# Kernel optimization log

Measured on AMD Instinct MI355X. Metric: run time of the kernel, lower is better.

The kernel has to match this reference:

```python
import jax, jax.numpy as jnp
import numpy as np
from jax import lax

NUM_HEAD = 16; M = 2; N = 2; RP = 16; HNR = 8; WNR = 8; NUM_RATIO = 64
ED = 4096           # origin_embed_dim == resize_embed_dim
HD = 4              # head dim (= ED / (NUM_HEAD * 64))
R = 1024 // RP      # 64
THETA = 10.0


def conv2d(x, w, b, stride, pad):
    y = lax.conv_general_dilated(x, w, (stride, stride), ((pad, pad), (pad, pad)),
                                 dimension_numbers=('NCHW', 'OIHW', 'NCHW'))
    return y + b[None, :, None, None]


def layernorm(x, g, b):
    mu = jnp.mean(x, -1, keepdims=True)
    var = jnp.mean((x - mu) ** 2, -1, keepdims=True)
    return (x - mu) * lax.rsqrt(var + 1e-5) * g + b


def l2norm(x):
    n = jnp.sqrt(jnp.sum(x * x, -1, keepdims=True))
    return x / jnp.maximum(n, 1e-12)


def window_partition(x, m, n):
    B, C, H, W = x.shape
    Hp = ((H + m - 1) // m) * m
    Wp = ((W + n - 1) // n) * n
    x = jnp.pad(x, ((0, 0), (0, 0), (0, Hp - H), (0, Wp - W)))
    wh, ww = Hp // m, Wp // n
    x = x.reshape(B, C, m, wh, n, ww).transpose(0, 2, 4, 1, 3, 5).reshape(B * m * n, C, wh, ww)
    return x, (wh, ww), (Hp, Wp)


def window_reverse(x, m, n, paged_shape):
    Hp, Wp = paged_shape
    Bmn, C, wh, ww = x.shape
    B = Bmn // (m * n)
    return x.reshape(B, m, n, C, wh, ww).transpose(0, 3, 1, 4, 2, 5).reshape(B, C, Hp, Wp)


def rope_rotate(t, h, w, theta):
    # 2D axial RoPE over a (h, w) grid flattened row-major; head dim split
    # half for the h-axis and half for the w-axis, consecutive-pair rotation.
    d = t.shape[-1]; dh = d // 2
    freqs = 1.0 / (theta ** (jnp.arange(0, dh, 2, dtype=jnp.float32) / dh))
    px = jnp.repeat(jnp.arange(h, dtype=jnp.float32), w)
    py = jnp.tile(jnp.arange(w, dtype=jnp.float32), h)
    ang = jnp.concatenate([px[:, None] * freqs, py[:, None] * freqs], -1)  # (h*w, dh)
    cos, sin = jnp.cos(ang), jnp.sin(ang)
    tp = t.reshape(t.shape[:-1] + (dh, 2))
    tr = jnp.stack([tp[..., 0] * cos - tp[..., 1] * sin,
                    tp[..., 0] * sin + tp[..., 1] * cos], -1)
    return tr.reshape(t.shape)


def setup_inputs() -> dict:
    key = jax.random.key(0)
    ks = jax.random.split(key, 12)
    s = 0.05
    inp = {
        'x': jax.random.normal(ks[0], (1, 3, 8, 8), jnp.float32),
        'x_conv_w': jax.random.normal(ks[1], (64, 3, 3, 3), jnp.float32) * s,
        'x_conv_b': jnp.zeros((64,), jnp.float32),
        'r_conv_w': jax.random.normal(ks[2], (64, 3, 3, 3), jnp.float32) * s,
        'r_conv_b': jnp.zeros((64,), jnp.float32),
        'patch_w': jax.random.normal(ks[3], (ED, 64, RP, RP), jnp.float32) * s,
        'patch_b': jnp.zeros((ED,), jnp.float32),
        'b_proj_w': jax.random.normal(ks[4], (HD, HD), jnp.float32) * 0.5,
        'b_proj_b': jnp.zeros((HD,), jnp.float32),
        'q_proj_w': jax.random.normal(ks[5], (HD, HD), jnp.float32) * 0.5,
        'q_proj_b': jnp.zeros((HD,), jnp.float32),
        'norm_b_g': jnp.ones((HD,), jnp.float32),
        'norm_b_b': jnp.zeros((HD,), jnp.float32),
        'norm_q_g': jnp.ones((HD,), jnp.float32),
        'norm_q_b': jnp.zeros((HD,), jnp.float32),
        'q_attn_w': jax.random.normal(ks[6], (1, HD), jnp.float32) * 0.5,
        'q_attn_b': jnp.zeros((1,), jnp.float32),
        'pos': jax.random.normal(ks[7], (1, NUM_HEAD, 65536, HD), jnp.float32),
        'proj_w': jax.random.normal(ks[8], (ED, ED, 1, 1), jnp.float32) * s,
        'proj_b': jnp.zeros((ED,), jnp.float32),
    }
    return inp


def reference(x, x_conv_w, x_conv_b, r_conv_w, r_conv_b, patch_w, patch_b,
              b_proj_w, b_proj_b, q_proj_w, q_proj_b,
              norm_b_g, norm_b_b, norm_q_g, norm_q_b,
              q_attn_w, q_attn_b, pos, proj_w, proj_b):
    B, C, H, W = x.shape
    x_feat = conv2d(x, x_conv_w, x_conv_b, 1, 1)                     # (B,64,H,W)
    x_win, xws, x_shape = window_partition(x_feat, M, N)
    pad_h, pad_w = x_shape[0] - H, x_shape[1] - W
    xp = jnp.pad(x, ((0, 0), (0, 0), (0, pad_h), (0, pad_w)))
    res_x = jax.image.resize(xp, (B, 3, 1024, 1024), method='bilinear')
    res_x = conv2d(res_x, r_conv_w, r_conv_b, 1, 1)                  # (B,64,1024,1024)
    res_x_base = conv2d(res_x, patch_w, patch_b, RP, 0)              # (B,4096,64,64)
    C_idx = ED // NUM_RATIO                                          # 64
    rxr = res_x_base.reshape(B, C_idx, HNR, WNR, R, R)
    rxr = rxr.transpose(0, 1, 4, 2, 5, 3).reshape(B, C_idx, R * HNR, R * WNR)  # (B,64,512,512)
    rx_win, rws, rx_shape = window_partition(rxr, M, N)              # (B*4,64,256,256)
    xw = x_win.reshape(B * M * N, NUM_HEAD, -1, xws[0] * xws[1]).swapaxes(-2, -1)  # (B*4,16,Nb,4)
    rw = rx_win.reshape(B * M * N, NUM_HEAD, -1, rws[0] * rws[1]).swapaxes(-2, -1) # (B*4,16,Nq,4)
    b = layernorm(xw, norm_b_g, norm_b_b) @ b_proj_w.T + b_proj_b
    q = layernorm(rw, norm_q_g, norm_q_b) @ q_proj_w.T + q_proj_b
    b_norm = l2norm(b)
    gate = jax.nn.sigmoid(q @ q_attn_w.T + q_attn_b)                 # (B*4,16,Nq,1)
    q = l2norm(q * gate + pos * (1.0 - gate))
    q_rot = rope_rotate(q, rws[0], rws[1], THETA)
    b_rot = rope_rotate(b_norm, xws[0], xws[1], THETA)
    attn = jnp.einsum('bhqd,bhkd->bhqk', q_rot, b_rot)               # (B*4,16,Nq,Nb)
    out_win = attn @ b                                               # (B*4,16,Nq,4)
    out_win = out_win.swapaxes(-2, -1).reshape(B * M * N, -1, rws[0], rws[1])
    n_x = window_reverse(out_win, M, N, rx_shape)                    # (B,64,512,512)
    n_x = n_x.reshape(B, C_idx, R, HNR, R, WNR).transpose(0, 1, 3, 5, 2, 4).reshape(B, -1, R, R)
    x_final = conv2d(n_x + res_x_base, proj_w, proj_b, 1, 0)         # (B,4096,64,64)
    return (x_final, attn)
```

## Files before the change

### kernel.cpp

```cpp
#include <hip/hip_runtime.h>
#include <hip/hip_bf16.h>
#include <math.h>
#include <cstddef>

#define CB_F     2097152ull
#define BIASC_F  4194304ull
#define BBUF_F   4198400ull
#define BROT_F   4202496ull
#define P_F      4206592ull
#define PB_F     20983808ull
#define PRWB_F   29372416ull
#define ATTN_OFF 16777216ull

typedef __attribute__((ext_vector_type(8))) short bf16x8;
typedef __attribute__((ext_vector_type(4))) float f32x4;

#define GLOAD16(gsrc, ldst) \
  __builtin_amdgcn_global_load_lds((const __attribute__((address_space(1))) void*)(gsrc), \
                                   (__attribute__((address_space(3))) void*)(ldst), 16, 0, 0)

__global__ __launch_bounds__(256) void k_xmap_bchain(
    const float* __restrict__ x, __hip_bfloat16* __restrict__ Xmb,
    const float* __restrict__ xcw, const float* __restrict__ xcb,
    const float* __restrict__ bpw, const float* __restrict__ bpb,
    const float* __restrict__ nbg, const float* __restrict__ nbb,
    float* __restrict__ b_buf, float* __restrict__ b_rot)
{
    __shared__ float xs[3][8][8];
    int t = threadIdx.x;
    if (t < 192) xs[t / 64][(t / 8) % 8][t % 8] = x[t];
    __syncthreads();

    if (blockIdx.x < 4096) {
        int s = blockIdx.x, py = s >> 6, px = s & 63;
        __hip_bfloat16 out4[4];
        #pragma unroll
        for (int u = 0; u < 4; ++u) {
            int k = t * 4 + u;
            float val = 0.0f;
            if (k < 972) {
                int ci = k / 324, r = k % 324, m = r / 18, n = r % 18;
                int row = 16 * py + m - 1, col = 16 * px + n - 1;
                if (row >= 0 && row < 1024 && col >= 0 && col < 1024) {
                    float fu = (row + 0.5f) * 0.0078125f - 0.5f;
                    float fv = (col + 0.5f) * 0.0078125f - 0.5f;
                    float fi = floorf(fu), fj = floorf(fv);
                    float tu = fu - fi, tv = fv - fj;
                    int i0 = (int)fi, j0 = (int)fj;
                    int i0c = min(max(i0, 0), 7), i1c = min(max(i0 + 1, 0), 7);
                    int j0c = min(max(j0, 0), 7), j1c = min(max(j0 + 1, 0), 7);
                    val = (xs[ci][i0c][j0c] * (1.f - tv) + xs[ci][i0c][j1c] * tv) * (1.f - tu)
                        + (xs[ci][i1c][j0c] * (1.f - tv) + xs[ci][i1c][j1c] * tv) * tu;
                }
            }
            out4[u] = __float2bfloat16(val);
        }
        *(ushort4*)(Xmb + (size_t)s * 1024 + t * 4) = *(const ushort4*)out4;
        return;
    }

    __shared__ float xf[64][8][8];
    for (int o = t; o < 4096; o += 256) {
        int c = o >> 6, i = (o >> 3) & 7, j = o & 7;
        float acc = xcb[c];
        for (int ic = 0; ic < 3; ++ic)
            for (int ky = 0; ky < 3; ++ky)
                for (int kx = 0; kx < 3; ++kx) {
                    int ii = i - 1 + ky, jj = j - 1 + kx;
                    if (ii >= 0 && ii < 8 && jj >= 0 && jj < 8)
                        acc = fmaf(xs[ic][ii][jj], xcw[((c * 3 + ic) * 3 + ky) * 3 + kx], acc);
                }
        xf[c][i][j] = acc;
    }
    __syncthreads();
    for (int idx = t; idx < 1024; idx += 256) {
        int wi = idx >> 8, h = (idx >> 4) & 15, pp = idx & 15;
        int pr = pp >> 2, pc = pp & 3;
        int gi = 4 * (wi >> 1) + pr, gj = 4 * (wi & 1) + pc;
        float v[4];
        #pragma unroll
        for (int d = 0; d < 4; ++d) v[d] = xf[h * 4 + d][gi][gj];
        float mu = 0.25f * (v[0] + v[1] + v[2] + v[3]);
        float var = 0.25f * ((v[0]-mu)*(v[0]-mu) + (v[1]-mu)*(v[1]-mu) +
                             (v[2]-mu)*(v[2]-mu) + (v[3]-mu)*(v[3]-mu));
        float inv = rsqrtf(var + 1e-5f);
        float xh[4];
        #pragma unroll
        for (int d = 0; d < 4; ++d) xh[d] = (v[d] - mu) * inv * nbg[d] + nbb[d];
        float bv[4];
        #pragma unroll
        for (int d = 0; d < 4; ++d) {
            float a = bpb[d];
            #pragma unroll
            for (int e = 0; e < 4; ++e) a = fmaf(xh[e], bpw[d * 4 + e], a);
            bv[d] = a;
        }
        #pragma unroll
        for (int d = 0; d < 4; ++d) b_buf[idx * 4 + d] = bv[d];
        float nn = sqrtf(bv[0]*bv[0] + bv[1]*bv[1] + bv[2]*bv[2] + bv[3]*bv[3]);
        float in2 = 1.0f / fmaxf(nn, 1e-12f);
        float bn[4];
        #pragma unroll
        for (int d = 0; d < 4; ++d) bn[d] = bv[d] * in2;
        float s0, c0, s1, c1;
        sincosf((float)pr, &s0, &c0);
        sincosf((float)pc, &s1, &c1);
        b_rot[idx * 4 + 0] = bn[0] * c0 - bn[1] * s0;
        b_rot[idx * 4 + 1] = bn[0] * s0 + bn[1] * c0;
        b_rot[idx * 4 + 2] = bn[2] * c1 - bn[3] * s1;
        b_rot[idx * 4 + 3] = bn[2] * s1 + bn[3] * c1;
    }
}

__global__ __launch_bounds__(256) void k_cmat(
    const float* __restrict__ pw, const float* __restrict__ rcw,
    const float* __restrict__ pb, const float* __restrict__ rcb,
    __hip_bfloat16* __restrict__ Cb, float* __restrict__ biasc)
{
    __shared__ __attribute__((aligned(16))) float Dz[20 * 20 * 28];
    __shared__ float red[256];
    int co = blockIdx.x;
    const float* pwc = pw + (size_t)co * 16384;
    int t = threadIdx.x;

    for (int i = t; i < 11200; i += 256) Dz[i] = 0.0f;

    float D[27] = {};
    float bsum = 0.0f;
    #pragma unroll 2
    for (int c = 0; c < 64; ++c) {
        float v = pwc[c * 256 + t];
        bsum = fmaf(rcb[c], v, bsum);
        #pragma unroll
        for (int j = 0; j < 27; ++j)
            D[j] = fmaf(rcw[c * 27 + j], v, D[j]);
    }
    __syncthreads();

    {
        int r = t >> 4, s = t & 15;
        float* dst = &Dz[((r + 2) * 20 + (s + 2)) * 28];
        #pragma unroll
        for (int q = 0; q < 6; ++q)
            *(f32x4*)(dst + q * 4) = *(const f32x4*)(D + q * 4);
        dst[24] = D[24]; dst[25] = D[25]; dst[26] = D[26];
    }
    red[t] = bsum;
    __syncthreads();

    if (t < 162) {
        int m = t / 9, n0 = (t % 9) * 2;
        float a0[3] = {}, a1[3] = {};
        #pragma unroll
        for (int ci = 0; ci < 3; ++ci)
            #pragma unroll
            for (int ky = 0; ky < 3; ++ky)
                #pragma unroll
                for (int kx = 0; kx < 3; ++kx) {
                    int j = ci * 9 + ky * 3 + kx;
                    const float* p = &Dz[((m - ky + 2) * 20 + (n0 - kx + 2)) * 28 + j];
                    a0[ci] += p[0];
                    a1[ci] += p[28];
                }
        size_t cb = (size_t)co * 1024;
        #pragma unroll
        for (int ci = 0; ci < 3; ++ci) {
            Cb[cb + ci * 324 + m * 18 + n0]     = __float2bfloat16(a0[ci]);
            Cb[cb + ci * 324 + m * 18 + n0 + 1] = __float2bfloat16(a1[ci]);
        }
    }
    if (t >= 162 && t < 214) Cb[(size_t)co * 1024 + 972 + (t - 162)] = __float2bfloat16(0.0f);

    for (int off = 128; off; off >>= 1) {
        __syncthreads();
        if (t < off) red[t] += red[t + off];
    }
    if (t == 0) biasc[co] = pb[co] + red[0];
}

__global__ __launch_bounds__(256) void k_cast_bf16(
    const float* __restrict__ in, __hip_bfloat16* __restrict__ out, long n)
{
    long i = ((long)blockIdx.x * 256 + threadIdx.x) * 8;
    if (i >= n) return;
    float4 v0 = *(const float4*)(in + i);
    float4 v1 = *(const float4*)(in + i + 4);
    __hip_bfloat16 h[8] = {__float2bfloat16(v0.x), __float2bfloat16(v0.y),
                           __float2bfloat16(v0.z), __float2bfloat16(v0.w),
                           __float2bfloat16(v1.x), __float2bfloat16(v1.y),
                           __float2bfloat16(v1.z), __float2bfloat16(v1.w)};
    *(ushort4*)(out + i)     = *(const ushort4*)h;
    *(ushort4*)(out + i + 4) = *(const ushort4*)(h + 4);
}

template <int BIASROW>
__global__ __launch_bounds__(512) void gemm_8p(
    const __hip_bfloat16* __restrict__ A, const __hip_bfloat16* __restrict__ B,
    const float* __restrict__ bias, float* __restrict__ C,
    int M, int N, int K)
{
    __shared__ short lds[65536];
    const short* Ag = (const short*)A;
    const short* Bg = (const short*)B;
    int t = threadIdx.x;
    int lane = t & 63;
    int wid = t >> 6;
    int wm = wid >> 2, wn = wid & 3;

    int nwg = gridDim.x * gridDim.y;
    int flat = blockIdx.y * gridDim.x + blockIdx.x;
    int swz = (flat & 7) * (nwg >> 3) + (flat >> 3);
    int bx = swz % gridDim.x, by = swz / gridDim.x;
    int m0 = by * 256, n0 = bx * 256;
    int T = K >> 6;

    int srow = t >> 3;
    int sc = ((t & 7) ^ (srow & 7)) * 8;
    const short* Asrc[4]; const short* Bsrc[4];
    #pragma unroll
    for (int p = 0; p < 4; ++p) {
        Asrc[p] = Ag + (size_t)(m0 + p * 64 + srow) * K + sc;
        Bsrc[p] = Bg + (size_t)(n0 + p * 64 + srow) * K + sc;
    }

    f32x4 acc[8][4] = {};

    #pragma unroll
    for (int u = 0; u < 2; ++u) {
        short* bA = lds + u * 32768;
        short* bB = bA + 16384;
        size_t ko = (size_t)u * 64;
        #pragma unroll
        for (int p = 0; p < 4; ++p) GLOAD16(Asrc[p] + ko, bA + p * 4096 + t * 8);
        #pragma unroll
        for (int p = 0; p < 4; ++p) GLOAD16(Bsrc[p] + ko, bB + p * 4096 + t * 8);
    }

    for (int tt = 0; tt < T; ++tt) {
        if (tt + 1 < T) { asm volatile("s_waitcnt vmcnt(8)" ::: "memory"); }
        else            { asm volatile("s_waitcnt vmcnt(0)" ::: "memory"); }
        __builtin_amdgcn_s_barrier();
        __builtin_amdgcn_sched_barrier(0);

        const char* Asb = (const char*)(lds + (tt & 1) * 32768);
        const char* Bsb = Asb + 32768;
        short* pA = lds + (tt & 1) * 32768;
        short* pB = pA + 16384;
        bool pf = (tt + 2) < T;
        size_t ko = (size_t)(tt + 2) * 64;

        bf16x8 af[4][2], bfr[4][2];
        #pragma unroll
        for (int f = 0; f < 4; ++f) {
            int r = wm * 128 + f * 16 + (lane & 15);
            #pragma unroll
            for (int ks = 0; ks < 2; ++ks) {
                int cb = ks * 64 + (lane >> 4) * 16;
                af[f][ks] = *(const bf16x8*)(Asb + r * 128 + (cb ^ ((r & 7) << 4)));
            }
        }
        #pragma unroll
        for (int g = 0; g < 2; ++g) {
            int r = wn * 64 + g * 16 + (lane & 15);
            #pragma unroll
            for (int ks = 0; ks < 2; ++ks) {
                int cb = ks * 64 + (lane >> 4) * 16;
                bfr[g][ks] = *(const bf16x8*)(Bsb + r * 128 + (cb ^ ((r & 7) << 4)));
            }
        }
        __builtin_amdgcn_s_barrier();
        __builtin_amdgcn_s_setprio(1);
        #pragma unroll
        for (int f = 0; f < 4; ++f)
            #pragma unroll
            for (int g = 0; g < 2; ++g)
                #pragma unroll
                for (int ks = 0; ks < 2; ++ks)
                    acc[f][g] = __builtin_amdgcn_mfma_f32_16x16x32_bf16(
                        af[f][ks], bfr[g][ks], acc[f][g], 0, 0, 0);
        __builtin_amdgcn_s_setprio(0);
        __builtin_amdgcn_s_barrier();
        #pragma unroll
        for (int g = 2; g < 4; ++g) {
            int r = wn * 64 + g * 16 + (lane & 15);
            #pragma unroll
            for (int ks = 0; ks < 2; ++ks) {
                int cb = ks * 64 + (lane >> 4) * 16;
                bfr[g][ks] = *(const bf16x8*)(Bsb + r * 128 + (cb ^ ((r & 7) << 4)));
            }
        }
        __builtin_amdgcn_s_barrier();
        __builtin_amdgcn_s_setprio(1);
        #pragma unroll
        for (int f = 0; f < 4; ++f)
            #pragma unroll
            for (int g = 2; g < 4; ++g)
                #pragma unroll
                for (int ks = 0; ks < 2; ++ks)
                    acc[f][g] = __builtin_amdgcn_mfma_f32_16x16x32_bf16(
                        af[f][ks], bfr[g][ks], acc[f][g], 0, 0, 0);
        __builtin_amdgcn_s_setprio(0);
        __builtin_amdgcn_s_barrier();
        #pragma unroll
        for (int f = 0; f < 4; ++f) {
            int r = wm * 128 + 64 + f * 16 + (lane & 15);
            #pragma unroll
            for (int ks = 0; ks < 2; ++ks) {
                int cb = ks * 64 + (lane >> 4) * 16;
                af[f][ks] = *(const bf16x8*)(Asb + r * 128 + (cb ^ ((r & 7) << 4)));
            }
        }
        if (pf) {
            #pragma unroll
            for (int p = 0; p < 4; ++p) GLOAD16(Bsrc[p] + ko, pB + p * 4096 + t * 8);
        }
        __builtin_amdgcn_s_barrier();
        __builtin_amdgcn_s_setprio(1);
        #pragma unroll
        for (int f = 0; f < 4; ++f)
            #pragma unroll
            for (int g = 0; g < 2; ++g)
                #pragma unroll
                for (int ks = 0; ks < 2; ++ks)
                    acc[4 + f][g] = __builtin_amdgcn_mfma_f32_16x16x32_bf16(
                        af[f][ks], bfr[g][ks], acc[4 + f][g], 0, 0, 0);
        __builtin_amdgcn_s_setprio(0);
        __builtin_amdgcn_s_barrier();
        if (pf) {
            #pragma unroll
            for (int p = 0; p < 4; ++p) GLOAD16(Asrc[p] + ko, pA + p * 4096 + t * 8);
        }
        __builtin_amdgcn_s_setprio(1);
        #pragma unroll
        for (int f = 0; f < 4; ++f)
            #pragma unroll
            for (int g = 2; g < 4; ++g)
                #pragma unroll
                for (int ks = 0; ks < 2; ++ks)
                    acc[4 + f][g] = __builtin_amdgcn_mfma_f32_16x16x32_bf16(
                        af[f][ks], bfr[g][ks], acc[4 + f][g], 0, 0, 0);
        __builtin_amdgcn_s_setprio(0);
    }

    #pragma unroll
    for (int f = 0; f < 8; ++f) {
        #pragma unroll
        for (int g = 0; g < 4; ++g) {
            int col = n0 + wn * 64 + g * 16 + (lane & 15);
            #pragma unroll
            for (int rg = 0; rg < 4; ++rg) {
                int row = m0 + wm * 128 + f * 16 + (lane >> 4) * 4 + rg;
                float bb = BIASROW ? bias[row] : bias[col];
                C[(size_t)row * N + col] = acc[f][g][rg] + bb;
            }
        }
    }
}

__global__ __launch_bounds__(256) void k_attn(
    const float* __restrict__ P, const float* __restrict__ b_buf, const float* __restrict__ b_rot,
    const float* __restrict__ qpw, const float* __restrict__ qpb,
    const float* __restrict__ nqg, const float* __restrict__ nqb,
    const float* __restrict__ qaw, const float* __restrict__ qab,
    const float* __restrict__ pos, __hip_bfloat16* __restrict__ Pb,
    float* __restrict__ attn_out)
{
    __shared__ float bs[16][4], brs[16][4];
    int t = threadIdx.x;
    int wh = blockIdx.y;
    int wi = wh >> 4, h = wh & 15;
    if (t < 64) {
        ((float*)bs)[t]  = b_buf[wh * 64 + t];
        ((float*)brs)[t] = b_rot[wh * 64 + t];
    }
    __syncthreads();
    int p = blockIdx.x * 256 + t;
    int wr = p >> 8, wc = p & 255;
    int gr = ((wi >> 1) << 8) + wr, gc = ((wi & 1) << 8) + wc;
    int y = gr >> 3, hnr = gr & 7, xq = gc >> 3, wnr = gc & 7;
    size_t base = (size_t)(y * 64 + xq) * 4096 + h * 256 + hnr * 8 + wnr;
    float r[4];
    #pragma unroll
    for (int d = 0; d < 4; ++d) r[d] = P[base + (size_t)d * 64];
    float mu = 0.25f * (r[0] + r[1] + r[2] + r[3]);
    float var = 0.25f * ((r[0]-mu)*(r[0]-mu) + (r[1]-mu)*(r[1]-mu) +
                         (r[2]-mu)*(r[2]-mu) + (r[3]-mu)*(r[3]-mu));
    float inv = rsqrtf(var + 1e-5f);
    float xh[4];
    #pragma unroll
    for (int d = 0; d < 4; ++d) xh[d] = (r[d] - mu) * inv * nqg[d] + nqb[d];
    float q4[4];
    #pragma unroll
    for (int d = 0; d < 4; ++d) {
        float a = qpb[d];
        #pragma unroll
        for (int e = 0; e < 4; ++e) a = fmaf(xh[e], qpw[d * 4 + e], a);
        q4[d] = a;
    }
    float z = qab[0];
    #pragma unroll
    for (int d = 0; d < 4; ++d) z = fmaf(q4[d], qaw[d], z);
    float gate = 1.0f / (1.0f + expf(-z));
    float4 pv = *(const float4*)(pos + ((size_t)h * 65536 + p) * 4);
    float v[4];
    v[0] = q4[0] * gate + pv.x * (1.0f - gate);
    v[1] = q4[1] * gate + pv.y * (1.0f - gate);
    v[2] = q4[2] * gate + pv.z * (1.0f - gate);
    v[3] = q4[3] * gate + pv.w * (1.0f - gate);
    float nn = sqrtf(v[0]*v[0] + v[1]*v[1] + v[2]*v[2] + v[3]*v[3]);
    float in2 = 1.0f / fmaxf(nn, 1e-12f);
    #pragma unroll
    for (int d = 0; d < 4; ++d) v[d] *= in2;
    float s0, c0, s1, c1;
    sincosf((float)wr, &s0, &c0);
    sincosf((float)wc, &s1, &c1);
    float qr[4];
    qr[0] = v[0] * c0 - v[1] * s0;
    qr[1] = v[0] * s0 + v[1] * c0;
    qr[2] = v[2] * c1 - v[3] * s1;
    qr[3] = v[2] * s1 + v[3] * c1;
    float arow[16];
    #pragma unroll
    for (int k = 0; k < 16; ++k)
        arow[k] = qr[0] * brs[k][0] + qr[1] * brs[k][1] + qr[2] * brs[k][2] + qr[3] * brs[k][3];
    size_t abase = ((size_t)wh * 65536 + p) * 16;
    #pragma unroll
    for (int kq = 0; kq < 4; ++kq) {
        float4 av;
        av.x = arow[kq * 4 + 0]; av.y = arow[kq * 4 + 1];
        av.z = arow[kq * 4 + 2]; av.w = arow[kq * 4 + 3];
        *(float4*)(attn_out + abase + kq * 4) = av;
    }
    float o[4] = {0.f, 0.f, 0.f, 0.f};
    #pragma unroll
    for (int k = 0; k < 16; ++k) {
        #pragma unroll
        for (int d = 0; d < 4; ++d) o[d] = fmaf(arow[k], bs[k][d], o[d]);
    }
    #pragma unroll
    for (int d = 0; d < 4; ++d)
        Pb[base + (size_t)d * 64] = __float2bfloat16(r[d] + o[d]);
}

extern "C" void kernel_launch(void* const* d_in, const int* in_sizes, int n_in,
                              void* d_out, int out_size, void* d_ws, size_t ws_size,
                              hipStream_t stream)
{
    (void)in_sizes; (void)n_in; (void)out_size; (void)ws_size;
    const float* x    = (const float*)d_in[0];
    const float* xcw  = (const float*)d_in[1];
    const float* xcb  = (const float*)d_in[2];
    const float* rcw  = (const float*)d_in[3];
    const float* rcb  = (const float*)d_in[4];
    const float* pw   = (const float*)d_in[5];
    const float* pb   = (const float*)d_in[6];
    const float* bpw  = (const float*)d_in[7];
    const float* bpb  = (const float*)d_in[8];
    const float* qpw  = (const float*)d_in[9];
    const float* qpb  = (const float*)d_in[10];
    const float* nbg  = (const float*)d_in[11];
    const float* nbb  = (const float*)d_in[12];
    const float* nqg  = (const float*)d_in[13];
    const float* nqb  = (const float*)d_in[14];
    const float* qaw  = (const float*)d_in[15];
    const float* qab  = (const float*)d_in[16];
    const float* pos  = (const float*)d_in[17];
    const float* prw  = (const float*)d_in[18];
    const float* prb  = (const float*)d_in[19];

    float* ws = (float*)d_ws;
    __hip_bfloat16* Xmb   = (__hip_bfloat16*)d_ws;
    __hip_bfloat16* Cb    = (__hip_bfloat16*)(ws + CB_F);
    float*          biasc = ws + BIASC_F;
    float*          b_buf = ws + BBUF_F;
    float*          b_rot = ws + BROT_F;
    float*          P     = ws + P_F;
    __hip_bfloat16* Pb    = (__hip_bfloat16*)(ws + PB_F);
    __hip_bfloat16* prwb  = (__hip_bfloat16*)(ws + PRWB_F);
    float* out = (float*)d_out;

    k_xmap_bchain<<<4097, 256, 0, stream>>>(x, Xmb, xcw, xcb, bpw, bpb, nbg, nbb,
                                            b_buf, b_rot);
    k_cmat<<<4096, 256, 0, stream>>>(pw, rcw, pb, rcb, Cb, biasc);
    gemm_8p<0><<<dim3(16, 16), 512, 0, stream>>>(Xmb, Cb, biasc, P, 4096, 4096, 1024);
    k_attn<<<dim3(256, 64), 256, 0, stream>>>(P, b_buf, b_rot, qpw, qpb, nqg, nqb,
                                              qaw, qab, pos, Pb, out + ATTN_OFF);
    k_cast_bf16<<<8192, 256, 0, stream>>>(prw, prwb, 16777216L);
    gemm_8p<1><<<dim3(16, 16), 512, 0, stream>>>(prwb, Pb, prb, out, 4096, 4096, 4096);
}
```

Measured before the change: 493.5 us.

## Process four output channels per block in k_cmat with LDS-staged weights

```diff
diff --git a/kernel.cpp b/kernel.cpp
--- a/kernel.cpp
+++ b/kernel.cpp
@@ -117,65 +117,86 @@
     const float* __restrict__ pb, const float* __restrict__ rcb,
     __hip_bfloat16* __restrict__ Cb, float* __restrict__ biasc)
 {
+    __shared__ __attribute__((aligned(16))) float Ws[64 * 28];
     __shared__ __attribute__((aligned(16))) float Dz[20 * 20 * 28];
-    __shared__ float red[256];
-    int co = blockIdx.x;
+    int t = threadIdx.x;
+    int w = t >> 6, lane = t & 63;
+    int co = blockIdx.x * 4 + w;
     const float* pwc = pw + (size_t)co * 16384;
-    int t = threadIdx.x;
-
+
+    for (int i = t; i < 1728; i += 256) Ws[(i / 27) * 28 + (i % 27)] = rcw[i];
+    if (t < 64) Ws[t * 28 + 27] = rcb[t];
     for (int i = t; i < 11200; i += 256) Dz[i] = 0.0f;
-
-    float D[27] = {};
+    __syncthreads();
+
+    float D[4][27];
+    #pragma unroll
+    for (int q = 0; q < 4; ++q)
+        #pragma unroll
+        for (int j = 0; j < 27; ++j) D[q][j] = 0.0f;
     float bsum = 0.0f;
-    #pragma unroll 2
+    const float* src = pwc + 4 * lane;
+    #pragma unroll 4
     for (int c = 0; c < 64; ++c) {
-        float v = pwc[c * 256 + t];
-        bsum = fmaf(rcb[c], v, bsum);
-        #pragma unroll
-        for (int j = 0; j < 27; ++j)
-            D[j] = fmaf(rcw[c * 27 + j], v, D[j]);
-    }
-    __syncthreads();
-
-    {
-        int r = t >> 4, s = t & 15;
-        float* dst = &Dz[((r + 2) * 20 + (s + 2)) * 28];
-        #pragma unroll
-        for (int q = 0; q < 6; ++q)
-            *(f32x4*)(dst + q * 4) = *(const f32x4*)(D + q * 4);
-        dst[24] = D[24]; dst[25] = D[25]; dst[26] = D[26];
-    }
-    red[t] = bsum;
-    __syncthreads();
-
-    if (t < 162) {
-        int m = t / 9, n0 = (t % 9) * 2;
-        float a0[3] = {}, a1[3] = {};
-        #pragma unroll
-        for (int ci = 0; ci < 3; ++ci)
-            #pragma unroll
-            for (int ky = 0; ky < 3; ++ky)
+        f32x4 v = *(const f32x4*)(src + c * 256);
+        const f32x4* wp = (const f32x4*)&Ws[c * 28];
+        #pragma unroll
+        for (int q7 = 0; q7 < 7; ++q7) {
+            f32x4 wv = wp[q7];
+            #pragma unroll
+            for (int e = 0; e < 4; ++e) {
+                int j = q7 * 4 + e;
+                if (j < 27) {
+                    #pragma unroll
+                    for (int q = 0; q < 4; ++q)
+                        D[q][j] = fmaf(wv[e], v[q], D[q][j]);
+                } else {
+                    bsum = fmaf(wv[e], v[0] + v[1] + v[2] + v[3], bsum);
+                }
+            }
+        }
+    }
+    #pragma unroll
+    for (int s = 32; s; s >>= 1) bsum += __shfl_down(bsum, s, 64);
+    if (lane == 0) biasc[co] = pb[co] + bsum;
+
+    for (int p = 0; p < 4; ++p) {
+        __syncthreads();
+        if (w == p) {
+            #pragma unroll
+            for (int q = 0; q < 4; ++q) {
+                int rs = 4 * lane + q, r = rs >> 4, s2 = rs & 15;
+                float* dst = &Dz[((r + 2) * 20 + (s2 + 2)) * 28];
                 #pragma unroll
-                for (int kx = 0; kx < 3; ++kx) {
-                    int j = ci * 9 + ky * 3 + kx;
-                    const float* p = &Dz[((m - ky + 2) * 20 + (n0 - kx + 2)) * 28 + j];
-                    a0[ci] += p[0];
-                    a1[ci] += p[28];
-                }
-        size_t cb = (size_t)co * 1024;
-        #pragma unroll
-        for (int ci = 0; ci < 3; ++ci) {
-            Cb[cb + ci * 324 + m * 18 + n0]     = __float2bfloat16(a0[ci]);
-            Cb[cb + ci * 324 + m * 18 + n0 + 1] = __float2bfloat16(a1[ci]);
-        }
-    }
-    if (t >= 162 && t < 214) Cb[(size_t)co * 1024 + 972 + (t - 162)] = __float2bfloat16(0.0f);
-
-    for (int off = 128; off; off >>= 1) {
+                for (int j = 0; j < 27; ++j) dst[j] = D[q][j];
+            }
+        }
         __syncthreads();
-        if (t < off) red[t] += red[t + off];
-    }
-    if (t == 0) biasc[co] = pb[co] + red[0];
+        int cop = blockIdx.x * 4 + p;
+        if (t < 162) {
+            int m = t / 9, n0 = (t % 9) * 2;
+            float a0[3] = {}, a1[3] = {};
+            #pragma unroll
+            for (int ci = 0; ci < 3; ++ci)
+                #pragma unroll
+                for (int ky = 0; ky < 3; ++ky)
+                    #pragma unroll
+                    for (int kx = 0; kx < 3; ++kx) {
+                        int j = ci * 9 + ky * 3 + kx;
+                        const float* pz = &Dz[((m - ky + 2) * 20 + (n0 - kx + 2)) * 28 + j];
+                        a0[ci] += pz[0];
+                        a1[ci] += pz[28];
+                    }
+            size_t cb = (size_t)cop * 1024;
+            #pragma unroll
+            for (int ci = 0; ci < 3; ++ci) {
+                Cb[cb + ci * 324 + m * 18 + n0]     = __float2bfloat16(a0[ci]);
+                Cb[cb + ci * 324 + m * 18 + n0 + 1] = __float2bfloat16(a1[ci]);
+            }
+        }
+        if (t >= 162 && t < 214)
+            Cb[(size_t)cop * 1024 + 972 + (t - 162)] = __float2bfloat16(0.0f);
+    }
 }
 
 __global__ __launch_bounds__(256) void k_cast_bf16(
@@ -481,7 +502,7 @@
 
     k_xmap_bchain<<<4097, 256, 0, stream>>>(x, Xmb, xcw, xcb, bpw, bpb, nbg, nbb,
                                             b_buf, b_rot);
-    k_cmat<<<4096, 256, 0, stream>>>(pw, rcw, pb, rcb, Cb, biasc);
+    k_cmat<<<1024, 256, 0, stream>>>(pw, rcw, pb, rcb, Cb, biasc);
     gemm_8p<0><<<dim3(16, 16), 512, 0, stream>>>(Xmb, Cb, biasc, P, 4096, 4096, 1024);
     k_attn<<<dim3(256, 64), 256, 0, stream>>>(P, b_buf, b_rot, qpw, qpb, nqg, nqb,
                                               qaw, qab, pos, Pb, out + ATTN_OFF);
```

Measured after the change: 492.7 us. Within noise of the previous version (-0.2%).
